# Optimization experiments

Measured on AMD Instinct MI355X. Metric: run time of the kernel, lower is better.

The kernel has to match this reference:

```python
import jax, jax.numpy as jnp
import numpy as np

N = 50000; E = 800000; F_IN = 165; HID = 32; H1 = 8; H3 = 4; OUT = 2
D1 = H1 * HID  # 256
D3 = H3 * HID  # 128
BN_EPS = 1e-5


def _gat_conv(x, edge_index, W, a_s, a_d, b, heads, add_self_loops):
    n = x.shape[0]
    if add_self_loops:
        loops = jnp.arange(n, dtype=edge_index.dtype)
        edge_index = jnp.concatenate([edge_index, jnp.stack([loops, loops])], axis=1)
    src, dst = edge_index[0], edge_index[1]
    h = (x @ W).reshape(n, heads, -1)                      # [N, H, D]
    a_src = jnp.sum(h * a_s, axis=-1)                      # [N, H]
    a_dst = jnp.sum(h * a_d, axis=-1)                      # [N, H]
    e = jax.nn.leaky_relu(a_src[src] + a_dst[dst], 0.2)    # [E, H] per-edge logits
    m = jax.ops.segment_max(e, dst, num_segments=n)        # segment-softmax over incoming edges
    ex = jnp.exp(e - m[dst])
    den = jax.ops.segment_sum(ex, dst, num_segments=n)
    alpha = ex / (den[dst] + 1e-16)                        # PyG softmax eps
    out = jax.ops.segment_sum(h[src] * alpha[:, :, None], dst, num_segments=n)
    return out.reshape(n, -1) + b                          # concat heads + bias


def _bn(x, g, b, mean, var):  # eval-mode BatchNorm1d
    return (x - mean) * jax.lax.rsqrt(var + BN_EPS) * g + b


def setup_inputs() -> dict:
    key = jax.random.key(0)
    ks = jax.random.split(key, 24)
    rn = lambda i, shape, s=0.05: jax.random.normal(ks[i], shape, dtype=jnp.float32) * s
    d = {}
    d["x"] = jax.random.normal(ks[0], (N, F_IN), dtype=jnp.float32)
    d["edge_index"] = jax.random.randint(ks[1], (2, E), 0, N, dtype=jnp.int32)
    d["W1"] = rn(2, (F_IN, D1)); d["a1s"] = rn(3, (H1, HID)); d["a1d"] = rn(4, (H1, HID))
    d["b1"] = jnp.zeros((D1,), jnp.float32)
    d["g1"] = jnp.ones((D1,), jnp.float32); d["be1"] = jnp.zeros((D1,), jnp.float32)
    d["m1"] = rn(5, (D1,)); d["v1"] = jax.random.uniform(ks[6], (D1,), minval=0.5, maxval=1.5)
    d["W2"] = rn(7, (D1, D1)); d["a2s"] = rn(8, (H1, HID)); d["a2d"] = rn(9, (H1, HID))
    d["b2"] = jnp.zeros((D1,), jnp.float32)
    d["g2"] = jnp.ones((D1,), jnp.float32); d["be2"] = jnp.zeros((D1,), jnp.float32)
    d["m2"] = rn(10, (D1,)); d["v2"] = jax.random.uniform(ks[11], (D1,), minval=0.5, maxval=1.5)
    d["W3"] = rn(12, (D1, D3)); d["a3s"] = rn(13, (H3, HID)); d["a3d"] = rn(14, (H3, HID))
    d["b3"] = jnp.zeros((D3,), jnp.float32)
    d["fcW"] = rn(15, (D3, OUT)); d["fcb"] = jnp.zeros((OUT,), jnp.float32)
    d["skW"] = rn(16, (F_IN, D3)); d["skb"] = jnp.zeros((D3,), jnp.float32)
    d["temp"] = jnp.array(1.0, jnp.float32)
    return d


def reference(x, edge_index, W1, a1s, a1d, b1, g1, be1, m1, v1,
              W2, a2s, a2d, b2, g2, be2, m2, v2,
              W3, a3s, a3d, b3, fcW, fcb, skW, skb, temp):
    x_init = x @ skW + skb                                   # skip Linear
    h = jax.nn.elu(_bn(_gat_conv(x, edge_index, W1, a1s, a1d, b1, H1, False), g1, be1, m1, v1))
    h = jax.nn.elu(_bn(_gat_conv(h, edge_index, W2, a2s, a2d, b2, H1, True), g2, be2, m2, v2) + h)
    h = _gat_conv(h * temp, edge_index, W3, a3s, a3d, b3, H3, True)
    return jax.nn.log_softmax((h + x_init) @ fcW + fcb, axis=1)
```

## Files before the change

### kernel.cpp

```cpp
#include <hip/hip_runtime.h>
#include <hip/hip_bf16.h>
#include <math.h>

#define N_NODES 50000
#define MP      50048
#define N_EDGES 800000
#define F_IN    165
#define KPAD1   192
#define D1      256
#define D3      128
#define CAP     64

typedef __attribute__((ext_vector_type(8))) short short8;
typedef __attribute__((ext_vector_type(4))) float floatx4;
typedef __attribute__((ext_vector_type(2))) float floatx2;

__device__ __forceinline__ float bflo(unsigned u) { return __uint_as_float(u << 16); }
__device__ __forceinline__ float bfhi(unsigned u) { return __uint_as_float(u & 0xffff0000u); }

__device__ __forceinline__ void fma8p(floatx2* a, float wgt, const uint4& v) {
    floatx2 w2; w2.x = wgt; w2.y = wgt;
    floatx2 p;
    p.x = bflo(v.x); p.y = bfhi(v.x); a[0] += w2 * p;
    p.x = bflo(v.y); p.y = bfhi(v.y); a[1] += w2 * p;
    p.x = bflo(v.z); p.y = bfhi(v.z); a[2] += w2 * p;
    p.x = bflo(v.w); p.y = bfhi(v.w); a[3] += w2 * p;
}

#if defined(__has_builtin)
#if __has_builtin(__builtin_amdgcn_global_load_lds)
#define HAS_GLL 1
#endif
#endif

__device__ __forceinline__ void gload16(const void* g, void* lds) {
#ifdef HAS_GLL
    __builtin_amdgcn_global_load_lds(
        (const __attribute__((address_space(1))) unsigned*)g,
        (__attribute__((address_space(3))) unsigned*)lds, 16, 0, 0);
#else
    *(int4*)lds = *(const int4*)g;
#endif
}

__global__ void prep_all(const float* __restrict__ x, __hip_bfloat16* __restrict__ xb,
                         const float* __restrict__ W1, __hip_bfloat16* __restrict__ Wt1,
                         const float* __restrict__ skW, __hip_bfloat16* __restrict__ skWt,
                         const float* __restrict__ W2, __hip_bfloat16* __restrict__ Wt2,
                         const float* __restrict__ W3, __hip_bfloat16* __restrict__ Wt3)
{
    const long long S0 = (long long)MP * KPAD1;
    const long long S1 = S0 + D1 * KPAD1;
    const long long S2 = S1 + D3 * KPAD1;
    const long long S3 = S2 + D1 * D1;
    const long long S4 = S3 + D3 * D1;
    long long idx = (long long)blockIdx.x * 256 + threadIdx.x;
    if (idx < S0) {
        const int m = idx / KPAD1, k = idx - (long long)m * KPAD1;
        xb[idx] = __float2bfloat16((k < F_IN && m < N_NODES) ? x[(size_t)m * F_IN + k] : 0.f);
    } else if (idx < S1) {
        const long long i = idx - S0;
        const int n = i / KPAD1, k = i - (long long)n * KPAD1;
        Wt1[i] = __float2bfloat16((k < F_IN) ? W1[(size_t)k * D1 + n] : 0.f);
    } else if (idx < S2) {
        const long long i = idx - S1;
        const int n = i / KPAD1, k = i - (long long)n * KPAD1;
        skWt[i] = __float2bfloat16((k < F_IN) ? skW[(size_t)k * D3 + n] : 0.f);
    } else if (idx < S3) {
        const long long i = idx - S2;
        const int n = i / D1, k = i - (long long)n * D1;
        Wt2[i] = __float2bfloat16(W2[(size_t)k * D1 + n]);
    } else if (idx < S4) {
        const long long i = idx - S3;
        const int n = i / D1, k = i - (long long)n * D1;
        Wt3[i] = __float2bfloat16(W3[(size_t)k * D3 + n]);
    }
}

__global__ __launch_bounds__(256) void gemm_bf16(
    const __hip_bfloat16* __restrict__ A, const __hip_bfloat16* __restrict__ Bt,
    const float* __restrict__ bias, const float* __restrict__ alphap,
    __hip_bfloat16* __restrict__ Cb, int M, int Ka, int NN, int NNb,
    __hip_bfloat16* __restrict__ Cx, const float* __restrict__ biasx)
{
    __shared__ short As[128 * 32];
    __shared__ short Bs[128 * 32];
    const int t  = threadIdx.x;
    const int m0 = blockIdx.x * 128;
    const int n0 = blockIdx.y * 128;
    const int w  = t >> 6, l = t & 63;
    const int wy = w >> 1, wx = w & 1;
    const int lm = l & 15, quad = l >> 4;
    const float alpha = alphap ? alphap[0] : 1.f;

    floatx4 acc[4][4] = {};

    const int ch0 = w * 128 + l;
    const int ch1 = ch0 + 64;
    const int r0a = ch0 >> 2, k0a = (ch0 & 3) * 8;
    const int r1a = ch1 >> 2, k1a = (ch1 & 3) * 8;

    for (int k0 = 0; k0 < Ka; k0 += 32) {
        gload16(A  + (size_t)(m0 + r0a) * Ka + k0 + k0a, &As[ch0 * 8]);
        gload16(A  + (size_t)(m0 + r1a) * Ka + k0 + k1a, &As[ch1 * 8]);
        gload16(Bt + (size_t)(n0 + r0a) * Ka + k0 + k0a, &Bs[ch0 * 8]);
        gload16(Bt + (size_t)(n0 + r1a) * Ka + k0 + k1a, &Bs[ch1 * 8]);
        __syncthreads();

        short8 af[4], bf[4];
#pragma unroll
        for (int i = 0; i < 4; ++i) {
            af[i] = *(const short8*)&As[(wy * 64 + i * 16 + lm) * 32 + quad * 8];
            bf[i] = *(const short8*)&Bs[(wx * 64 + i * 16 + lm) * 32 + quad * 8];
        }
#pragma unroll
        for (int mi = 0; mi < 4; ++mi)
#pragma unroll
            for (int ni = 0; ni < 4; ++ni)
                acc[mi][ni] = __builtin_amdgcn_mfma_f32_16x16x32_bf16(
                    af[mi], bf[ni], acc[mi][ni], 0, 0, 0);
        __syncthreads();
    }

#pragma unroll
    for (int mi = 0; mi < 4; ++mi) {
#pragma unroll
        for (int r = 0; r < 4; ++r) {
            const int gm = m0 + wy * 64 + mi * 16 + quad * 4 + r;
            if (gm >= M) continue;
#pragma unroll
            for (int ni = 0; ni < 4; ++ni) {
                const int gn = n0 + wx * 64 + ni * 16 + lm;
                float v = acc[mi][ni][r] * alpha;
                if (gn < NNb) {
                    if (bias) v += bias[gn];
                    Cb[(size_t)gm * NNb + gn] = __float2bfloat16(v);
                } else {
                    v += biasx[gn - NNb];
                    Cx[(size_t)gm * (NN - NNb) + gn - NNb] = __float2bfloat16(v);
                }
            }
        }
    }
}

__global__ void attn_prep(const __hip_bfloat16* __restrict__ h, const float* __restrict__ a_s,
                          const float* __restrict__ a_d, float* __restrict__ osrc,
                          float* __restrict__ odst, int Nn, int hshift)
{
    const int H   = 1 << hshift;
    const int gid = blockIdx.x * blockDim.x + threadIdx.x;
    if (gid >= Nn * H) return;
    const int n  = gid >> hshift;
    const int hh = gid & (H - 1);
    const uint4* hp = (const uint4*)(h + (size_t)n * (H * 32) + hh * 32);
    const float* ap = a_s + hh * 32;
    const float* bp = a_d + hh * 32;
    float s1 = 0.f, s2 = 0.f;
#pragma unroll
    for (int c = 0; c < 4; ++c) {
        const uint4 v = hp[c];
        const unsigned uu[4] = {v.x, v.y, v.z, v.w};
#pragma unroll
        for (int j = 0; j < 4; ++j) {
            const int d = c * 8 + j * 2;
            const float e0 = bflo(uu[j]), e1 = bfhi(uu[j]);
            s1 += e0 * ap[d] + e1 * ap[d + 1];
            s2 += e0 * bp[d] + e1 * bp[d + 1];
        }
    }
    osrc[gid] = s1;
    odst[gid] = s2;
}

__global__ void deg_hist(const int* __restrict__ ei, int* __restrict__ deg, int E)
{
    const int e = blockIdx.x * blockDim.x + threadIdx.x;
    if (e < E) atomicAdd(&deg[ei[E + e]], 1);
}

__global__ __launch_bounds__(1024) void scan_rowptr(const int* __restrict__ deg,
                                                    int* __restrict__ rowptr, int n)
{
    __shared__ int sums[1024];
    const int tid = threadIdx.x;
    const int chunk = (n + 1023) / 1024;
    const int lo = tid * chunk;
    const int hi = min(lo + chunk, n);
    int s = 0;
    for (int i = lo; i < hi; ++i) s += deg[i];
    sums[tid] = s;
    __syncthreads();
    for (int off = 1; off < 1024; off <<= 1) {
        int t = 0;
        if (tid >= off) t = sums[tid - off];
        __syncthreads();
        if (tid >= off) sums[tid] += t;
        __syncthreads();
    }
    int run = sums[tid] - s;
    for (int i = lo; i < hi; ++i) { rowptr[i] = run; run += deg[i]; }
    if (lo < n && hi == n) rowptr[n] = run;
}

__global__ void csr_fill(const int* __restrict__ ei, const int* __restrict__ rowptr,
                         int* __restrict__ cursor, int* __restrict__ csr_src, int E)
{
    const int e = blockIdx.x * blockDim.x + threadIdx.x;
    if (e >= E) return;
    const int dst = ei[E + e];
    const int pos = rowptr[dst] + atomicAdd(&cursor[dst], 1);
    csr_src[pos] = ei[e];
}

template <int HSH, int D, int POST>
__global__ __launch_bounds__(256) void gat_gather_v9(
    const __hip_bfloat16* __restrict__ h, const float* __restrict__ asrc,
    const float* __restrict__ adst, const int* __restrict__ rowptr,
    const int* __restrict__ csr_src, int selfloop,
    const float* __restrict__ bias, const float* __restrict__ g,
    const float* __restrict__ be, const float* __restrict__ mean,
    const float* __restrict__ var, const __hip_bfloat16* __restrict__ residB,
    const float* __restrict__ fcW, const float* __restrict__ fcb,
    float* __restrict__ outF, __hip_bfloat16* __restrict__ outB)
{
    constexpr int H    = 1 << HSH;
    constexpr int LPE  = D / 8;
    constexpr int EPW  = 64 / LPE;
    constexpr int SUBS = 64 >> HSH;
    constexpr int MAXJ = CAP / SUBS;

    const int w = threadIdx.x >> 6, l = threadIdx.x & 63;
    const int node = blockIdx.x * 4 + w;

    __shared__ float sW[4][CAP * H];
    __shared__ int   sSrc[4][CAP];

    const int r0  = rowptr[node];
    const int deg = rowptr[node + 1] - r0;
    const int tot = min(deg + selfloop, CAP);

    const int hh  = l & (H - 1);
    const int sub = l >> HSH;
    const float ad = adst[node * H + hh];

    float ex[MAXJ];
    float sum = 0.f;
    {
        int nj = 0;
        for (int e = sub; e < tot; e += SUBS, ++nj) {
            const int s = (e < deg) ? csr_src[r0 + e] : node;
            if (hh == 0) sSrc[w][e] = s;
            float v = asrc[s * H + hh] + ad;
            v = v > 0.f ? v : 0.2f * v;
            ex[nj] = __expf(v);
            sum += ex[nj];
        }
    }
#pragma unroll
    for (int off = H; off < 64; off <<= 1) sum += __shfl_xor(sum, off);
    const float rs = 1.f / (sum + 1e-16f);
    {
        int nj = 0;
        for (int e = sub; e < tot; e += SUBS, ++nj)
            sW[w][e * H + hh] = ex[nj] * rs;
    }

    const int sw   = l / LPE;
    const int lo   = l % LPE;
    const int dimb = lo * 8;
    const int hh2  = dimb >> 5;
    floatx2 a0[4] = {}, a1[4] = {};

    for (int e = sw; e < tot; e += 2 * EPW) {
        const int e2  = e + EPW;
        const bool v2 = e2 < tot;
        const int sa = sSrc[w][e];
        const int sb = v2 ? sSrc[w][e2] : node;
        const float wa = sW[w][e * H + hh2];
        const float wb = v2 ? sW[w][e2 * H + hh2] : 0.f;
        const uint4 qa = *(const uint4*)&h[(size_t)sa * D + dimb];
        const uint4 qb = *(const uint4*)&h[(size_t)sb * D + dimb];
        fma8p(a0, wa, qa);
        fma8p(a1, wb, qb);
    }
    float acc[8];
#pragma unroll
    for (int v = 0; v < 4; ++v) {
        const floatx2 s2v = a0[v] + a1[v];
        acc[v * 2] = s2v.x; acc[v * 2 + 1] = s2v.y;
    }
#pragma unroll
    for (int off = LPE; off < 64; off <<= 1)
#pragma unroll
        for (int v = 0; v < 8; ++v) acc[v] += __shfl_xor(acc[v], off);

    if (POST == 3) {
        float v0 = 0.f, v1 = 0.f;
        if (l < LPE) {
            const uint4 rv = *(const uint4*)&residB[(size_t)node * D + dimb];
            const float rr[8] = {bflo(rv.x), bfhi(rv.x), bflo(rv.y), bfhi(rv.y),
                                 bflo(rv.z), bfhi(rv.z), bflo(rv.w), bfhi(rv.w)};
#pragma unroll
            for (int v = 0; v < 8; ++v) {
                const float val = acc[v] + bias[dimb + v] + rr[v];
                v0 += val * fcW[(dimb + v) * 2 + 0];
                v1 += val * fcW[(dimb + v) * 2 + 1];
            }
        }
#pragma unroll
        for (int off = 1; off < LPE; off <<= 1) {
            v0 += __shfl_xor(v0, off);
            v1 += __shfl_xor(v1, off);
        }
        if (l == 0) {
            const float l0 = v0 + fcb[0], l1 = v1 + fcb[1];
            const float m2 = fmaxf(l0, l1);
            const float lse = m2 + logf(__expf(l0 - m2) + __expf(l1 - m2));
            outF[node * 2 + 0] = l0 - lse;
            outF[node * 2 + 1] = l1 - lse;
        }
    } else {
        if (l < LPE) {
            float rr[8] = {};
            if (POST == 2) {
                const uint4 rv = *(const uint4*)&residB[(size_t)node * D + dimb];
                rr[0] = bflo(rv.x); rr[1] = bfhi(rv.x);
                rr[2] = bflo(rv.y); rr[3] = bfhi(rv.y);
                rr[4] = bflo(rv.z); rr[5] = bfhi(rv.z);
                rr[6] = bflo(rv.w); rr[7] = bfhi(rv.w);
            }
            __hip_bfloat16 rb[8];
#pragma unroll
            for (int v = 0; v < 8; ++v) {
                const int f = dimb + v;
                float vv = acc[v] + bias[f];
                vv = (vv - mean[f]) * rsqrtf(var[f] + 1e-5f) * g[f] + be[f];
                if (POST == 2) vv += rr[v];
                vv = vv > 0.f ? vv : (__expf(vv) - 1.f);
                rb[v] = __float2bfloat16(vv);
            }
            *(uint4*)&outB[(size_t)node * D + dimb] = *(uint4*)&rb[0];
        }
    }
}

extern "C" void kernel_launch(void* const* d_in, const int* in_sizes, int n_in,
                              void* d_out, int out_size, void* d_ws, size_t ws_size,
                              hipStream_t stream)
{
    const float* x    = (const float*)d_in[0];
    const int*   ei   = (const int*)  d_in[1];
    const float* W1   = (const float*)d_in[2];
    const float* a1s  = (const float*)d_in[3];
    const float* a1d  = (const float*)d_in[4];
    const float* b1   = (const float*)d_in[5];
    const float* g1   = (const float*)d_in[6];
    const float* be1  = (const float*)d_in[7];
    const float* m1   = (const float*)d_in[8];
    const float* v1   = (const float*)d_in[9];
    const float* W2   = (const float*)d_in[10];
    const float* a2s  = (const float*)d_in[11];
    const float* a2d  = (const float*)d_in[12];
    const float* b2   = (const float*)d_in[13];
    const float* g2   = (const float*)d_in[14];
    const float* be2  = (const float*)d_in[15];
    const float* m2   = (const float*)d_in[16];
    const float* v2   = (const float*)d_in[17];
    const float* W3   = (const float*)d_in[18];
    const float* a3s  = (const float*)d_in[19];
    const float* a3d  = (const float*)d_in[20];
    const float* b3   = (const float*)d_in[21];
    const float* fcW  = (const float*)d_in[22];
    const float* fcb  = (const float*)d_in[23];
    const float* skW  = (const float*)d_in[24];
    const float* skb  = (const float*)d_in[25];
    const float* temp = (const float*)d_in[26];

    float* out = (float*)d_out;

    const int N = N_NODES, E = N_EDGES;

    float* ws = (float*)d_ws;
    size_t o = 0;
    float* asrc  = ws + o;  o += (size_t)N * 8;
    float* adst  = ws + o;  o += (size_t)N * 8;
    int* rowptr  = (int*)(ws + o);  o += N + 1;
    o = (o + 3) & ~(size_t)3;
    int* csr_src = (int*)(ws + o);  o += E;
    o = (o + 3) & ~(size_t)3;
    __hip_bfloat16* xb     = (__hip_bfloat16*)(ws + o); o += (size_t)MP * KPAD1 / 2;
    __hip_bfloat16* bufCb  = (__hip_bfloat16*)(ws + o); o += (size_t)MP * D1 / 2;
    __hip_bfloat16* hb     = (__hip_bfloat16*)(ws + o); o += (size_t)N * D1 / 2;
    __hip_bfloat16* xinitB = (__hip_bfloat16*)(ws + o); o += (size_t)N * D3 / 2;
    __hip_bfloat16* Wt1    = (__hip_bfloat16*)(ws + o); o += (size_t)D1 * KPAD1 / 2;
    __hip_bfloat16* skWt   = (__hip_bfloat16*)(ws + o); o += (size_t)D3 * KPAD1 / 2;
    __hip_bfloat16* Wt2    = (__hip_bfloat16*)(ws + o); o += (size_t)D1 * D1 / 2;
    __hip_bfloat16* Wt3    = (__hip_bfloat16*)(ws + o); o += (size_t)D3 * D1 / 2;
    int* deg    = (int*)hb;
    int* cursor = deg + N;

    const int MT128 = MP / 128;

    hipMemsetAsync(deg, 0, (size_t)2 * N * sizeof(int), stream);
    deg_hist<<<(E + 255) / 256, 256, 0, stream>>>(ei, deg, E);
    scan_rowptr<<<1, 1024, 0, stream>>>(deg, rowptr, N);
    csr_fill<<<(E + 255) / 256, 256, 0, stream>>>(ei, rowptr, cursor, csr_src, E);

    {
        const long long tote = (long long)MP * KPAD1 + (long long)D1 * KPAD1 +
                               (long long)D3 * KPAD1 + (long long)D1 * D1 + (long long)D3 * D1;
        prep_all<<<(tote + 255) / 256, 256, 0, stream>>>(x, xb, W1, Wt1, skW, skWt, W2, Wt2, W3, Wt3);
    }

    gemm_bf16<<<dim3(MT128, 3), 256, 0, stream>>>(xb, Wt1, nullptr, nullptr,
                                                  hb, N, KPAD1, D1 + D3, D1, xinitB, skb);
    attn_prep<<<(N * 8 + 255) / 256, 256, 0, stream>>>(hb, a1s, a1d, asrc, adst, N, 3);
    gat_gather_v9<3, D1, 1><<<N / 4, 256, 0, stream>>>(hb, asrc, adst, rowptr, csr_src, 0,
                                                       b1, g1, be1, m1, v1, nullptr, nullptr, nullptr,
                                                       nullptr, bufCb);

    gemm_bf16<<<dim3(MT128, 2), 256, 0, stream>>>(bufCb, Wt2, nullptr, nullptr,
                                                  hb, N, D1, D1, D1, nullptr, nullptr);
    attn_prep<<<(N * 8 + 255) / 256, 256, 0, stream>>>(hb, a2s, a2d, asrc, adst, N, 3);
    gat_gather_v9<3, D1, 2><<<N / 4, 256, 0, stream>>>(hb, asrc, adst, rowptr, csr_src, 1,
                                                       b2, g2, be2, m2, v2, bufCb, nullptr, nullptr,
                                                       nullptr, bufCb);

    gemm_bf16<<<dim3(MT128, 1), 256, 0, stream>>>(bufCb, Wt3, nullptr, temp,
                                                  hb, N, D1, D3, D3, nullptr, nullptr);
    attn_prep<<<(N * 4 + 255) / 256, 256, 0, stream>>>(hb, a3s, a3d, asrc, adst, N, 2);
    gat_gather_v9<2, D3, 3><<<N / 4, 256, 0, stream>>>(hb, asrc, adst, rowptr, csr_src, 1,
                                                       b3, nullptr, nullptr, nullptr, nullptr, xinitB,
                                                       fcW, fcb, out, nullptr);

    (void)in_sizes; (void)n_in; (void)out_size; (void)ws_size;
}
```

Baseline: 629.4 us.

## Fold attention vectors into weight matrices and drop attn_prep kernels

The per-head attention projections a_src and a_dst are precomputed as extra columns of the transposed weight matrices (W·a), so each GEMM emits the attention logits directly and the three attn_prep kernels go away. This removes the re-read of h and three launches. In exchange each GEMM launches an extra, mostly empty N-tile column (16 or 8 live columns out of 128). The logits are now computed from bf16-rounded folded weights rather than from bf16 h, which slightly changes numerics.

```diff
diff --git a/kernel.cpp b/kernel.cpp
--- a/kernel.cpp
+++ b/kernel.cpp
@@ -44,16 +44,24 @@
 }
 
 __global__ void prep_all(const float* __restrict__ x, __hip_bfloat16* __restrict__ xb,
-                         const float* __restrict__ W1, __hip_bfloat16* __restrict__ Wt1,
-                         const float* __restrict__ skW, __hip_bfloat16* __restrict__ skWt,
-                         const float* __restrict__ W2, __hip_bfloat16* __restrict__ Wt2,
-                         const float* __restrict__ W3, __hip_bfloat16* __restrict__ Wt3)
+                         const float* __restrict__ W1, const float* __restrict__ skW,
+                         const float* __restrict__ a1s, const float* __restrict__ a1d,
+                         __hip_bfloat16* __restrict__ Bt1,
+                         const float* __restrict__ W2,
+                         const float* __restrict__ a2s, const float* __restrict__ a2d,
+                         __hip_bfloat16* __restrict__ Bt2,
+                         const float* __restrict__ W3,
+                         const float* __restrict__ a3s, const float* __restrict__ a3d,
+                         __hip_bfloat16* __restrict__ Bt3)
 {
     const long long S0 = (long long)MP * KPAD1;
-    const long long S1 = S0 + D1 * KPAD1;
-    const long long S2 = S1 + D3 * KPAD1;
-    const long long S3 = S2 + D1 * D1;
-    const long long S4 = S3 + D3 * D1;
+    const long long S1 = S0 + 256 * KPAD1;
+    const long long S2 = S1 + 128 * KPAD1;
+    const long long S3 = S2 + 16 * KPAD1;
+    const long long S4 = S3 + 256 * D1;
+    const long long S5 = S4 + 16 * D1;
+    const long long S6 = S5 + 128 * D1;
+    const long long S7 = S6 + 8 * D1;
     long long idx = (long long)blockIdx.x * 256 + threadIdx.x;
     if (idx < S0) {
         const int m = idx / KPAD1, k = idx - (long long)m * KPAD1;
@@ -61,27 +69,58 @@
     } else if (idx < S1) {
         const long long i = idx - S0;
         const int n = i / KPAD1, k = i - (long long)n * KPAD1;
-        Wt1[i] = __float2bfloat16((k < F_IN) ? W1[(size_t)k * D1 + n] : 0.f);
+        Bt1[(size_t)n * KPAD1 + k] = __float2bfloat16((k < F_IN) ? W1[(size_t)k * D1 + n] : 0.f);
     } else if (idx < S2) {
         const long long i = idx - S1;
         const int n = i / KPAD1, k = i - (long long)n * KPAD1;
-        skWt[i] = __float2bfloat16((k < F_IN) ? skW[(size_t)k * D3 + n] : 0.f);
+        Bt1[(size_t)(256 + n) * KPAD1 + k] =
+            __float2bfloat16((k < F_IN) ? skW[(size_t)k * D3 + n] : 0.f);
     } else if (idx < S3) {
         const long long i = idx - S2;
-        const int n = i / D1, k = i - (long long)n * D1;
-        Wt2[i] = __float2bfloat16(W2[(size_t)k * D1 + n]);
+        const int r = i / KPAD1, k = i - (long long)r * KPAD1;
+        const int hh = r & 7;
+        const float* av = (r < 8) ? a1s : a1d;
+        float s = 0.f;
+        if (k < F_IN)
+#pragma unroll
+            for (int d = 0; d < 32; ++d) s += W1[(size_t)k * D1 + hh * 32 + d] * av[hh * 32 + d];
+        Bt1[(size_t)(384 + r) * KPAD1 + k] = __float2bfloat16(s);
     } else if (idx < S4) {
         const long long i = idx - S3;
         const int n = i / D1, k = i - (long long)n * D1;
-        Wt3[i] = __float2bfloat16(W3[(size_t)k * D3 + n]);
+        Bt2[(size_t)n * D1 + k] = __float2bfloat16(W2[(size_t)k * D1 + n]);
+    } else if (idx < S5) {
+        const long long i = idx - S4;
+        const int r = i / D1, k = i - (long long)r * D1;
+        const int hh = r & 7;
+        const float* av = (r < 8) ? a2s : a2d;
+        float s = 0.f;
+#pragma unroll
+        for (int d = 0; d < 32; ++d) s += W2[(size_t)k * D1 + hh * 32 + d] * av[hh * 32 + d];
+        Bt2[(size_t)(256 + r) * D1 + k] = __float2bfloat16(s);
+    } else if (idx < S6) {
+        const long long i = idx - S5;
+        const int n = i / D1, k = i - (long long)n * D1;
+        Bt3[(size_t)n * D1 + k] = __float2bfloat16(W3[(size_t)k * D3 + n]);
+    } else if (idx < S7) {
+        const long long i = idx - S6;
+        const int r = i / D1, k = i - (long long)r * D1;
+        const int hh = r & 3;
+        const float* av = (r < 4) ? a3s : a3d;
+        float s = 0.f;
+#pragma unroll
+        for (int d = 0; d < 32; ++d) s += W3[(size_t)k * D3 + hh * 32 + d] * av[hh * 32 + d];
+        Bt3[(size_t)(128 + r) * D1 + k] = __float2bfloat16(s);
     }
 }
 
 __global__ __launch_bounds__(256) void gemm_bf16(
     const __hip_bfloat16* __restrict__ A, const __hip_bfloat16* __restrict__ Bt,
-    const float* __restrict__ bias, const float* __restrict__ alphap,
-    __hip_bfloat16* __restrict__ Cb, int M, int Ka, int NN, int NNb,
-    __hip_bfloat16* __restrict__ Cx, const float* __restrict__ biasx)
+    const float* __restrict__ alphap,
+    __hip_bfloat16* __restrict__ Cb, int Dh,
+    __hip_bfloat16* __restrict__ Cx, const float* __restrict__ biasx, int Dx,
+    float* __restrict__ asrc, float* __restrict__ adst, int H,
+    int M, int Ka)
 {
     __shared__ short As[128 * 32];
     __shared__ short Bs[128 * 32];
@@ -92,6 +131,7 @@
     const int wy = w >> 1, wx = w & 1;
     const int lm = l & 15, quad = l >> 4;
     const float alpha = alphap ? alphap[0] : 1.f;
+    const int NNlive = Dh + Dx + 2 * H;
 
     floatx4 acc[4][4] = {};
 
@@ -131,46 +171,20 @@
 #pragma unroll
             for (int ni = 0; ni < 4; ++ni) {
                 const int gn = n0 + wx * 64 + ni * 16 + lm;
-                float v = acc[mi][ni][r] * alpha;
-                if (gn < NNb) {
-                    if (bias) v += bias[gn];
-                    Cb[(size_t)gm * NNb + gn] = __float2bfloat16(v);
+                if (gn >= NNlive) continue;
+                const float v = acc[mi][ni][r] * alpha;
+                if (gn < Dh) {
+                    Cb[(size_t)gm * Dh + gn] = __float2bfloat16(v);
+                } else if (gn < Dh + Dx) {
+                    Cx[(size_t)gm * Dx + gn - Dh] = __float2bfloat16(v + biasx[gn - Dh]);
                 } else {
-                    v += biasx[gn - NNb];
-                    Cx[(size_t)gm * (NN - NNb) + gn - NNb] = __float2bfloat16(v);
+                    const int c = gn - Dh - Dx;
+                    if (c < H) asrc[(size_t)gm * H + c] = v;
+                    else       adst[(size_t)gm * H + c - H] = v;
                 }
             }
         }
     }
-}
-
-__global__ void attn_prep(const __hip_bfloat16* __restrict__ h, const float* __restrict__ a_s,
-                          const float* __restrict__ a_d, float* __restrict__ osrc,
-                          float* __restrict__ odst, int Nn, int hshift)
-{
-    const int H   = 1 << hshift;
-    const int gid = blockIdx.x * blockDim.x + threadIdx.x;
-    if (gid >= Nn * H) return;
-    const int n  = gid >> hshift;
-    const int hh = gid & (H - 1);
-    const uint4* hp = (const uint4*)(h + (size_t)n * (H * 32) + hh * 32);
-    const float* ap = a_s + hh * 32;
-    const float* bp = a_d + hh * 32;
-    float s1 = 0.f, s2 = 0.f;
-#pragma unroll
-    for (int c = 0; c < 4; ++c) {
-        const uint4 v = hp[c];
-        const unsigned uu[4] = {v.x, v.y, v.z, v.w};
-#pragma unroll
-        for (int j = 0; j < 4; ++j) {
-            const int d = c * 8 + j * 2;
-            const float e0 = bflo(uu[j]), e1 = bfhi(uu[j]);
-            s1 += e0 * ap[d] + e1 * ap[d + 1];
-            s2 += e0 * bp[d] + e1 * bp[d + 1];
-        }
-    }
-    osrc[gid] = s1;
-    odst[gid] = s2;
 }
 
 __global__ void deg_hist(const int* __restrict__ ei, int* __restrict__ deg, int E)
@@ -393,10 +407,9 @@
     __hip_bfloat16* bufCb  = (__hip_bfloat16*)(ws + o); o += (size_t)MP * D1 / 2;
     __hip_bfloat16* hb     = (__hip_bfloat16*)(ws + o); o += (size_t)N * D1 / 2;
     __hip_bfloat16* xinitB = (__hip_bfloat16*)(ws + o); o += (size_t)N * D3 / 2;
-    __hip_bfloat16* Wt1    = (__hip_bfloat16*)(ws + o); o += (size_t)D1 * KPAD1 / 2;
-    __hip_bfloat16* skWt   = (__hip_bfloat16*)(ws + o); o += (size_t)D3 * KPAD1 / 2;
-    __hip_bfloat16* Wt2    = (__hip_bfloat16*)(ws + o); o += (size_t)D1 * D1 / 2;
-    __hip_bfloat16* Wt3    = (__hip_bfloat16*)(ws + o); o += (size_t)D3 * D1 / 2;
+    __hip_bfloat16* Bt1    = (__hip_bfloat16*)(ws + o); o += (size_t)512 * KPAD1 / 2;
+    __hip_bfloat16* Bt2    = (__hip_bfloat16*)(ws + o); o += (size_t)384 * D1 / 2;
+    __hip_bfloat16* Bt3    = (__hip_bfloat16*)(ws + o); o += (size_t)256 * D1 / 2;
     int* deg    = (int*)hb;
     int* cursor = deg + N;
 
@@ -408,28 +421,29 @@
     csr_fill<<<(E + 255) / 256, 256, 0, stream>>>(ei, rowptr, cursor, csr_src, E);
 
     {
-        const long long tote = (long long)MP * KPAD1 + (long long)D1 * KPAD1 +
-                               (long long)D3 * KPAD1 + (long long)D1 * D1 + (long long)D3 * D1;
-        prep_all<<<(tote + 255) / 256, 256, 0, stream>>>(x, xb, W1, Wt1, skW, skWt, W2, Wt2, W3, Wt3);
-    }
-
-    gemm_bf16<<<dim3(MT128, 3), 256, 0, stream>>>(xb, Wt1, nullptr, nullptr,
-                                                  hb, N, KPAD1, D1 + D3, D1, xinitB, skb);
-    attn_prep<<<(N * 8 + 255) / 256, 256, 0, stream>>>(hb, a1s, a1d, asrc, adst, N, 3);
+        const long long tote = (long long)MP * KPAD1 + (256 + 128 + 16) * (long long)KPAD1 +
+                               (256 + 16 + 128 + 8) * (long long)D1;
+        prep_all<<<(tote + 255) / 256, 256, 0, stream>>>(
+            x, xb, W1, skW, a1s, a1d, Bt1, W2, a2s, a2d, Bt2, W3, a3s, a3d, Bt3);
+    }
+
+    gemm_bf16<<<dim3(MT128, 4), 256, 0, stream>>>(xb, Bt1, nullptr,
+                                                  hb, D1, xinitB, skb, D3,
+                                                  asrc, adst, 8, N, KPAD1);
     gat_gather_v9<3, D1, 1><<<N / 4, 256, 0, stream>>>(hb, asrc, adst, rowptr, csr_src, 0,
                                                        b1, g1, be1, m1, v1, nullptr, nullptr, nullptr,
                                                        nullptr, bufCb);
 
-    gemm_bf16<<<dim3(MT128, 2), 256, 0, stream>>>(bufCb, Wt2, nullptr, nullptr,
-                                                  hb, N, D1, D1, D1, nullptr, nullptr);
-    attn_prep<<<(N * 8 + 255) / 256, 256, 0, stream>>>(hb, a2s, a2d, asrc, adst, N, 3);
+    gemm_bf16<<<dim3(MT128, 3), 256, 0, stream>>>(bufCb, Bt2, nullptr,
+                                                  hb, D1, nullptr, nullptr, 0,
+                                                  asrc, adst, 8, N, D1);
     gat_gather_v9<3, D1, 2><<<N / 4, 256, 0, stream>>>(hb, asrc, adst, rowptr, csr_src, 1,
                                                        b2, g2, be2, m2, v2, bufCb, nullptr, nullptr,
                                                        nullptr, bufCb);
 
-    gemm_bf16<<<dim3(MT128, 1), 256, 0, stream>>>(bufCb, Wt3, nullptr, temp,
-                                                  hb, N, D1, D3, D3, nullptr, nullptr);
-    attn_prep<<<(N * 4 + 255) / 256, 256, 0, stream>>>(hb, a3s, a3d, asrc, adst, N, 2);
+    gemm_bf16<<<dim3(MT128, 2), 256, 0, stream>>>(bufCb, Bt3, temp,
+                                                  hb, D3, nullptr, nullptr, 0,
+                                                  asrc, adst, 4, N, D1);
     gat_gather_v9<2, D3, 3><<<N / 4, 256, 0, stream>>>(hb, asrc, adst, rowptr, csr_src, 1,
                                                        b3, nullptr, nullptr, nullptr, nullptr, xinitB,
                                                        fcW, fcb, out, nullptr);
```

After: 617.3 us. No clear change (-1.9%).
